# Performance work log

Hardware: AMD Instinct MI355X
Metric: run time of the kernel (lower is better)

## Reference

```python
import jax, jax.numpy as jnp
import numpy as np

N_NODES = 50000
N_EDGES = 400000
NUM_FEATS = 128
LATENT_DIM_Y = 64
HIDDEN = 512
OUT = 2


def gcn_conv(x, edge_index, W, b, num_nodes):
    """PyG GCNConv: add self-loops, symmetric normalization, x @ W then scatter-add."""
    x = x @ W  # [N, out_ch]
    loop = jnp.arange(num_nodes)
    row = jnp.concatenate([edge_index[0], loop])  # source nodes
    col = jnp.concatenate([edge_index[1], loop])  # target nodes
    deg = jax.ops.segment_sum(jnp.ones_like(col, dtype=x.dtype), col, num_segments=num_nodes)
    dinv = jnp.where(deg > 0, jax.lax.rsqrt(deg), 0.0)
    norm = dinv[row] * dinv[col]  # [E+N]
    msgs = norm[:, None] * x[row]  # gather source features, scale
    out = jax.ops.segment_sum(msgs, col, num_segments=num_nodes)
    return out + b


def setup_inputs() -> dict:
    key = jax.random.key(0)
    k1, k2, k3, k4, k5, k6, k7 = jax.random.split(key, 7)
    in_ch = NUM_FEATS + LATENT_DIM_Y
    inputs = {
        "edge_index": jax.random.randint(k1, (2, N_EDGES), 0, N_NODES),
        "X": jax.random.normal(k2, (N_NODES, NUM_FEATS), dtype=jnp.float32),
        "u_Y": jax.random.normal(k3, (N_NODES, LATENT_DIM_Y), dtype=jnp.float32),
        "W1": jax.random.normal(k4, (in_ch, HIDDEN), dtype=jnp.float32) / np.sqrt(in_ch),
        "b1": jnp.zeros((HIDDEN,), dtype=jnp.float32),
        "W2": jax.random.normal(k5, (HIDDEN, OUT), dtype=jnp.float32) / np.sqrt(HIDDEN),
        "b2": jnp.zeros((OUT,), dtype=jnp.float32),
    }
    return inputs


def reference(edge_index, X, u_Y, W1, b1, W2, b2):
    latent = jnp.concatenate([u_Y, X], axis=1)  # [N, latent+feats]
    h = jax.nn.relu(gcn_conv(latent, edge_index, W1, b1, N_NODES))
    y = gcn_conv(h, edge_index, W2, b2, N_NODES)
    # nn.Softmax() on a 2D tensor defaults to dim=1
    return jax.nn.softmax(y, axis=1)
```

## Files before the change

kernel.cpp:

```cpp
#include <hip/hip_runtime.h>

#define N_NODES 50000
#define N_EDGES 400000
#define FEATS   128
#define LAT     64
#define IN_CH   192
#define HID     512
#define MB      64
#define CAP     32

#define E4       100000
#define SC_BLKS  391
#define CVT_BLKS 9375
#define W1_BLKS  384

typedef __attribute__((ext_vector_type(8))) short bf16x8;
typedef __attribute__((ext_vector_type(4))) float f32x4;

static inline int cdiv(int a, int b) { return (a + b - 1) / b; }

__device__ __forceinline__ unsigned short f2bf(float f) {
    unsigned int u = __float_as_uint(f);
    u = (u + 0x7fffu + ((u >> 16) & 1u)) >> 16;
    return (unsigned short)u;
}
__device__ __forceinline__ float bf_lo(unsigned int u) {
    return __uint_as_float(u << 16);
}
__device__ __forceinline__ float bf_hi(unsigned int u) {
    return __uint_as_float(u & 0xffff0000u);
}

__global__ __launch_bounds__(256) void
k_front(const int* __restrict__ ei, int* __restrict__ cursor, int* __restrict__ csr_src,
        const float* __restrict__ uY, const float* __restrict__ X,
        unsigned short* __restrict__ latent,
        const float* __restrict__ W1, unsigned short* __restrict__ W1f) {
    int bid = blockIdx.x;
    if (bid < SC_BLKS) {
        int i4 = bid * 256 + threadIdx.x;
        if (i4 < E4) {
            int4 r = ((const int4*)ei)[i4];
            int4 c = ((const int4*)(ei + N_EDGES))[i4];
            int p0 = atomicAdd(&cursor[c.x], 1);
            int p1 = atomicAdd(&cursor[c.y], 1);
            int p2 = atomicAdd(&cursor[c.z], 1);
            int p3 = atomicAdd(&cursor[c.w], 1);
            csr_src[c.x * CAP + p0] = r.x;
            csr_src[c.y * CAP + p1] = r.y;
            csr_src[c.z * CAP + p2] = r.z;
            csr_src[c.w * CAP + p3] = r.w;
        }
    } else if (bid < SC_BLKS + CVT_BLKS) {
        int idx = (bid - SC_BLKS) * 256 + threadIdx.x;
        int i = idx / 48, q = idx % 48;
        const float4* uY4 = (const float4*)uY;
        const float4* X4  = (const float4*)X;
        float4 v = (q < LAT / 4) ? uY4[i * (LAT / 4) + q]
                                 : X4[i * (FEATS / 4) + (q - LAT / 4)];
        uint2 o;
        o.x = (unsigned int)f2bf(v.x) | ((unsigned int)f2bf(v.y) << 16);
        o.y = (unsigned int)f2bf(v.z) | ((unsigned int)f2bf(v.w) << 16);
        ((uint2*)latent)[idx] = o;
    } else {
        int idx = (bid - SC_BLKS - CVT_BLKS) * 256 + threadIdx.x;
        if (idx < IN_CH * HID) {
            int k = idx / HID, n = idx % HID;
            int ntile = n >> 4, nn = n & 15;
            int kc = k >> 5, q = (k >> 3) & 3, j = k & 7;
            int dst = (((ntile * 6 + kc) * 64 + q * 16 + nn) << 3) + j;
            W1f[dst] = f2bf(W1[idx]);
        }
    }
}

__device__ __forceinline__ void load_row(uint4* a, const uint4* __restrict__ L4,
                                         int r, int l8) {
    const uint4* p = L4 + (size_t)r * 24 + l8 * 3;
    a[0] = p[0]; a[1] = p[1]; a[2] = p[2];
}
__device__ __forceinline__ void fma_row(float* acc, const uint4* a, float wt) {
#pragma unroll
    for (int i = 0; i < 3; ++i) {
        unsigned int u0 = a[i].x, u1 = a[i].y, u2 = a[i].z, u3 = a[i].w;
        acc[i * 8 + 0] = fmaf(wt, bf_lo(u0), acc[i * 8 + 0]);
        acc[i * 8 + 1] = fmaf(wt, bf_hi(u0), acc[i * 8 + 1]);
        acc[i * 8 + 2] = fmaf(wt, bf_lo(u1), acc[i * 8 + 2]);
        acc[i * 8 + 3] = fmaf(wt, bf_hi(u1), acc[i * 8 + 3]);
        acc[i * 8 + 4] = fmaf(wt, bf_lo(u2), acc[i * 8 + 4]);
        acc[i * 8 + 5] = fmaf(wt, bf_hi(u2), acc[i * 8 + 5]);
        acc[i * 8 + 6] = fmaf(wt, bf_lo(u3), acc[i * 8 + 6]);
        acc[i * 8 + 7] = fmaf(wt, bf_hi(u3), acc[i * 8 + 7]);
    }
}

__global__ __launch_bounds__(256) void
k_gather_agg(const int* __restrict__ cursor, const int* __restrict__ csr_src,
             const unsigned short* __restrict__ latent, unsigned short* __restrict__ agg) {
    int w    = blockIdx.x * 4 + (threadIdx.x >> 6);
    int lane = threadIdx.x & 63;
    if (w >= N_NODES) return;
    int qt = lane >> 3, l8 = lane & 7;
    const uint4* __restrict__ L4 = (const uint4*)latent;

    int jlo = w * CAP;
    int deg  = cursor[w];
    int rawe = csr_src[jlo + max(qt - 1, 0)];
    int raw2 = csr_src[jlo + qt + 7];
    int raw1 = (qt == 0) ? w : rawe;
    int r1 = min(max(raw1, 0), N_NODES - 1);
    int r2 = min(max(raw2, 0), N_NODES - 1);
    int d1 = cursor[r1];
    int d2 = cursor[r2];

    uint4 a[3];
    load_row(a, L4, r1, l8);

    float di = rsqrtf((float)(deg + 1));
    float w1 = (qt == 0) ? di
             : ((qt - 1 < deg) ? rsqrtf((float)(d1 + 1)) : 0.f);

    float acc[24];
#pragma unroll
    for (int i = 0; i < 24; ++i) acc[i] = 0.f;

    bool more = (deg > 7);
    uint4 b[3];
    if (more) load_row(b, L4, r2, l8);

    fma_row(acc, a, w1);
    if (more) {
        float w2 = (qt + 7 < deg) ? rsqrtf((float)(d2 + 1)) : 0.f;
        fma_row(acc, b, w2);
        for (int e = 15 + qt; e < deg; e += 8) {
            int r = csr_src[jlo + e];
            float wt = rsqrtf((float)(cursor[r] + 1));
            uint4 t[3];
            load_row(t, L4, r, l8);
            fma_row(acc, t, wt);
        }
    }

#pragma unroll
    for (int i = 0; i < 24; ++i) {
        acc[i] += __shfl_xor(acc[i], 8);
        acc[i] += __shfl_xor(acc[i], 16);
        acc[i] += __shfl_xor(acc[i], 32);
    }

    if (qt == 0) {
        uint4* op = (uint4*)agg + (size_t)w * 24 + l8 * 3;
#pragma unroll
        for (int v = 0; v < 3; ++v) {
            uint4 o;
            o.x = (unsigned int)f2bf(di * acc[v * 8 + 0]) |
                  ((unsigned int)f2bf(di * acc[v * 8 + 1]) << 16);
            o.y = (unsigned int)f2bf(di * acc[v * 8 + 2]) |
                  ((unsigned int)f2bf(di * acc[v * 8 + 3]) << 16);
            o.z = (unsigned int)f2bf(di * acc[v * 8 + 4]) |
                  ((unsigned int)f2bf(di * acc[v * 8 + 5]) << 16);
            o.w = (unsigned int)f2bf(di * acc[v * 8 + 6]) |
                  ((unsigned int)f2bf(di * acc[v * 8 + 7]) << 16);
            op[v] = o;
        }
    }
}

__global__ __launch_bounds__(256, 2) void
k_gemm_mfma(const unsigned short* __restrict__ agg, const unsigned short* __restrict__ W1f,
            const float* __restrict__ b1, const float* __restrict__ W2,
            float* __restrict__ y_pre) {
    __shared__ unsigned short Af[MB * IN_CH];
    __shared__ float red[4][MB][2];

    int t  = threadIdx.x;
    int m0 = blockIdx.x * MB;

    {
        const uint4* src = (const uint4*)agg;
        for (int idx = t; idx < MB * 24; idx += 256) {
            int row = idx / 24, c = idx % 24;
            int g = m0 + row;
            uint4 v = make_uint4(0u, 0u, 0u, 0u);
            if (g < N_NODES) v = src[(size_t)g * 24 + c];
            int mt = row >> 4, m = row & 15, kc = c >> 2, q = c & 3;
            ((uint4*)Af)[(mt * 6 + kc) * 64 + q * 16 + m] = v;
        }
    }
    __syncthreads();

    int wid = t >> 6, lane = t & 63;
    int nl = lane & 15, q = lane >> 4;

    float b1v[8], w2a[8], w2b[8];
#pragma unroll
    for (int nt = 0; nt < 8; ++nt) {
        int n = wid * 128 + nt * 16 + nl;
        b1v[nt] = b1[n];
        w2a[nt] = W2[n * 2 + 0];
        w2b[nt] = W2[n * 2 + 1];
    }

    f32x4 acc[4][8];
#pragma unroll
    for (int mt = 0; mt < 4; ++mt)
#pragma unroll
        for (int nt = 0; nt < 8; ++nt) acc[mt][nt] = (f32x4){0.f, 0.f, 0.f, 0.f};

    const bf16x8* Afv = (const bf16x8*)Af;
    const bf16x8* Bv  = (const bf16x8*)W1f;
#pragma unroll
    for (int kc = 0; kc < 6; ++kc) {
        bf16x8 a[4];
#pragma unroll
        for (int mt = 0; mt < 4; ++mt) a[mt] = Afv[(mt * 6 + kc) * 64 + lane];
#pragma unroll
        for (int nt = 0; nt < 8; ++nt) {
            bf16x8 b = Bv[((wid * 8 + nt) * 6 + kc) * 64 + lane];
#pragma unroll
            for (int mt = 0; mt < 4; ++mt)
                acc[mt][nt] = __builtin_amdgcn_mfma_f32_16x16x32_bf16(a[mt], b, acc[mt][nt], 0, 0, 0);
        }
    }

#pragma unroll
    for (int mt = 0; mt < 4; ++mt) {
#pragma unroll
        for (int r = 0; r < 4; ++r) {
            float p0 = 0.f, p1 = 0.f;
#pragma unroll
            for (int nt = 0; nt < 8; ++nt) {
                float h = fmaxf(acc[mt][nt][r] + b1v[nt], 0.f);
                p0 = fmaf(h, w2a[nt], p0);
                p1 = fmaf(h, w2b[nt], p1);
            }
#pragma unroll
            for (int off = 1; off < 16; off <<= 1) {
                p0 += __shfl_xor(p0, off);
                p1 += __shfl_xor(p1, off);
            }
            if (nl == 0) {
                int row = mt * 16 + q * 4 + r;
                red[wid][row][0] = p0;
                red[wid][row][1] = p1;
            }
        }
    }
    __syncthreads();
    if (t < MB * 2) {
        int row = t >> 1, j = t & 1;
        float s = red[0][row][j] + red[1][row][j] + red[2][row][j] + red[3][row][j];
        int g = m0 + row;
        if (g < N_NODES) y_pre[g * 2 + j] = s;
    }
}

__global__ __launch_bounds__(256) void
k_gather_y(const int* __restrict__ cursor, const int* __restrict__ csr_src,
           const float* __restrict__ y_pre, const float* __restrict__ b2,
           float* __restrict__ out) {
    int i  = blockIdx.x * 32 + (threadIdx.x >> 3);
    int l8 = threadIdx.x & 7;
    if (i >= N_NODES) return;
    const float2* __restrict__ yp = (const float2*)y_pre;

    int jlo = i * CAP;
    int deg  = cursor[i];
    int rawe = csr_src[jlo + max(l8 - 1, 0)];
    int raw2 = csr_src[jlo + l8 + 7];
    int raw1 = (l8 == 0) ? i : rawe;
    int r1 = min(max(raw1, 0), N_NODES - 1);
    int r2 = min(max(raw2, 0), N_NODES - 1);
    int d1 = cursor[r1], d2 = cursor[r2];
    float2 v1 = yp[r1];

    float di = rsqrtf((float)(deg + 1));
    float w1 = (l8 == 0) ? di
             : ((l8 - 1 < deg) ? rsqrtf((float)(d1 + 1)) : 0.f);
    float a0 = w1 * v1.x, a1 = w1 * v1.y;
    if (deg > 7) {
        float2 v2 = yp[r2];
        float w2 = (l8 + 7 < deg) ? rsqrtf((float)(d2 + 1)) : 0.f;
        a0 = fmaf(w2, v2.x, a0);
        a1 = fmaf(w2, v2.y, a1);
        for (int e = 15 + l8; e < deg; e += 8) {
            int r = csr_src[jlo + e];
            float wt = rsqrtf((float)(cursor[r] + 1));
            float2 v = yp[r];
            a0 = fmaf(wt, v.x, a0);
            a1 = fmaf(wt, v.y, a1);
        }
    }
#pragma unroll
    for (int off = 1; off < 8; off <<= 1) {
        a0 += __shfl_xor(a0, off);
        a1 += __shfl_xor(a1, off);
    }
    if (l8 == 0) {
        float ya = di * a0 + b2[0];
        float yb = di * a1 + b2[1];
        float mx = fmaxf(ya, yb);
        float e0 = expf(ya - mx);
        float e1 = expf(yb - mx);
        float inv = 1.0f / (e0 + e1);
        out[i * 2 + 0] = e0 * inv;
        out[i * 2 + 1] = e1 * inv;
    }
}


extern "C" void kernel_launch(void* const* d_in, const int* in_sizes, int n_in,
                              void* d_out, int out_size, void* d_ws, size_t ws_size,
                              hipStream_t stream) {
    const int*   ei = (const int*)d_in[0];
    const float* X  = (const float*)d_in[1];
    const float* uY = (const float*)d_in[2];
    const float* W1 = (const float*)d_in[3];
    const float* b1 = (const float*)d_in[4];
    const float* W2 = (const float*)d_in[5];
    const float* b2 = (const float*)d_in[6];
    float* out = (float*)d_out;

    char* ws = (char*)d_ws;
    auto carve = [&](size_t bytes) {
        char* p = ws;
        ws += (bytes + 255) & ~size_t(255);
        return p;
    };
    int*   cursor    = (int*)carve(N_NODES * sizeof(int));
    int*   csr_src   = (int*)carve((size_t)N_NODES * CAP * sizeof(int));
    unsigned short* latent = (unsigned short*)carve((size_t)N_NODES * IN_CH * 2);
    unsigned short* aggb   = (unsigned short*)carve((size_t)N_NODES * IN_CH * 2);
    unsigned short* W1f    = (unsigned short*)carve((size_t)IN_CH * HID * 2);
    float* y_pre     = (float*)carve((size_t)N_NODES * 2 * sizeof(float));

    hipMemsetAsync(cursor, 0, N_NODES * sizeof(int), stream);

    k_front     <<<SC_BLKS + CVT_BLKS + W1_BLKS, 256, 0, stream>>>(
                      ei, cursor, csr_src, uY, X, latent, W1, W1f);

    k_gather_agg<<<cdiv(N_NODES, 4), 256, 0, stream>>>(
                      cursor, csr_src, latent, aggb);

    k_gemm_mfma <<<cdiv(N_NODES, MB), 256, 0, stream>>>(aggb, W1f, b1, W2, y_pre);

    k_gather_y  <<<cdiv(N_NODES, 32), 256, 0, stream>>>(
                      cursor, csr_src, y_pre, b2, out);
}
```

Measured before the change: 186.9 us.

## Restructure neighbor aggregation as two half-wave streams with prefetched dword loads

The gather-aggregate kernel drops the layout of 8 lane-groups, each loading 3 uint4 per neighbor row. Instead each half-wave of 32 lanes reads a whole 192-feature row as coalesced dwords, and the two halves walk alternate neighbors. Neighbor indices and normalization weights are loaded once per lane and broadcast with shuffles, and the next row is prefetched while the current one is accumulated. This cuts the cross-lane reduction from 72 shuffles to 6, lowers register use and folds the destination scale into the edge weights. The cost is a longer serial chain of neighbor steps per half-wave, with narrower loads in flight per lane.

After: 175.6 us. 1.06x faster.

```diff
diff --git a/kernel.cpp b/kernel.cpp
--- a/kernel.cpp
+++ b/kernel.cpp
@@ -23,6 +23,9 @@
     unsigned int u = __float_as_uint(f);
     u = (u + 0x7fffu + ((u >> 16) & 1u)) >> 16;
     return (unsigned short)u;
+}
+__device__ __forceinline__ unsigned int pack2bf(float lo, float hi) {
+    return (unsigned int)f2bf(lo) | ((unsigned int)f2bf(hi) << 16);
 }
 __device__ __forceinline__ float bf_lo(unsigned int u) {
     return __uint_as_float(u << 16);
@@ -59,8 +62,8 @@
         float4 v = (q < LAT / 4) ? uY4[i * (LAT / 4) + q]
                                  : X4[i * (FEATS / 4) + (q - LAT / 4)];
         uint2 o;
-        o.x = (unsigned int)f2bf(v.x) | ((unsigned int)f2bf(v.y) << 16);
-        o.y = (unsigned int)f2bf(v.z) | ((unsigned int)f2bf(v.w) << 16);
+        o.x = pack2bf(v.x, v.y);
+        o.y = pack2bf(v.z, v.w);
         ((uint2*)latent)[idx] = o;
     } else {
         int idx = (bid - SC_BLKS - CVT_BLKS) * 256 + threadIdx.x;
@@ -74,95 +77,67 @@
     }
 }
 
-__device__ __forceinline__ void load_row(uint4* a, const uint4* __restrict__ L4,
-                                         int r, int l8) {
-    const uint4* p = L4 + (size_t)r * 24 + l8 * 3;
-    a[0] = p[0]; a[1] = p[1]; a[2] = p[2];
-}
-__device__ __forceinline__ void fma_row(float* acc, const uint4* a, float wt) {
-#pragma unroll
-    for (int i = 0; i < 3; ++i) {
-        unsigned int u0 = a[i].x, u1 = a[i].y, u2 = a[i].z, u3 = a[i].w;
-        acc[i * 8 + 0] = fmaf(wt, bf_lo(u0), acc[i * 8 + 0]);
-        acc[i * 8 + 1] = fmaf(wt, bf_hi(u0), acc[i * 8 + 1]);
-        acc[i * 8 + 2] = fmaf(wt, bf_lo(u1), acc[i * 8 + 2]);
-        acc[i * 8 + 3] = fmaf(wt, bf_hi(u1), acc[i * 8 + 3]);
-        acc[i * 8 + 4] = fmaf(wt, bf_lo(u2), acc[i * 8 + 4]);
-        acc[i * 8 + 5] = fmaf(wt, bf_hi(u2), acc[i * 8 + 5]);
-        acc[i * 8 + 6] = fmaf(wt, bf_lo(u3), acc[i * 8 + 6]);
-        acc[i * 8 + 7] = fmaf(wt, bf_hi(u3), acc[i * 8 + 7]);
-    }
-}
-
 __global__ __launch_bounds__(256) void
 k_gather_agg(const int* __restrict__ cursor, const int* __restrict__ csr_src,
              const unsigned short* __restrict__ latent, unsigned short* __restrict__ agg) {
     int w    = blockIdx.x * 4 + (threadIdx.x >> 6);
     int lane = threadIdx.x & 63;
     if (w >= N_NODES) return;
-    int qt = lane >> 3, l8 = lane & 7;
-    const uint4* __restrict__ L4 = (const uint4*)latent;
-
-    int jlo = w * CAP;
-    int deg  = cursor[w];
-    int rawe = csr_src[jlo + max(qt - 1, 0)];
-    int raw2 = csr_src[jlo + qt + 7];
-    int raw1 = (qt == 0) ? w : rawe;
-    int r1 = min(max(raw1, 0), N_NODES - 1);
-    int r2 = min(max(raw2, 0), N_NODES - 1);
-    int d1 = cursor[r1];
-    int d2 = cursor[r2];
-
-    uint4 a[3];
-    load_row(a, L4, r1, l8);
-
+    int h  = lane >> 5;
+    int il = lane & 31;
+    const unsigned int* __restrict__ L = (const unsigned int*)latent;
+
+    int deg = cursor[w];
+    int raw = csr_src[w * CAP + max(il - 1, 0)];
+    int rl  = (il == 0) ? w : min(max(raw, 0), N_NODES - 1);
+    int dl  = cursor[rl];
     float di = rsqrtf((float)(deg + 1));
-    float w1 = (qt == 0) ? di
-             : ((qt - 1 < deg) ? rsqrtf((float)(d1 + 1)) : 0.f);
-
-    float acc[24];
-#pragma unroll
-    for (int i = 0; i < 24; ++i) acc[i] = 0.f;
-
-    bool more = (deg > 7);
-    uint4 b[3];
-    if (more) load_row(b, L4, r2, l8);
-
-    fma_row(acc, a, w1);
-    if (more) {
-        float w2 = (qt + 7 < deg) ? rsqrtf((float)(d2 + 1)) : 0.f;
-        fma_row(acc, b, w2);
-        for (int e = 15 + qt; e < deg; e += 8) {
-            int r = csr_src[jlo + e];
-            float wt = rsqrtf((float)(cursor[r] + 1));
-            uint4 t[3];
-            load_row(t, L4, r, l8);
-            fma_row(acc, t, wt);
-        }
-    }
-
-#pragma unroll
-    for (int i = 0; i < 24; ++i) {
-        acc[i] += __shfl_xor(acc[i], 8);
-        acc[i] += __shfl_xor(acc[i], 16);
-        acc[i] += __shfl_xor(acc[i], 32);
-    }
-
-    if (qt == 0) {
-        uint4* op = (uint4*)agg + (size_t)w * 24 + l8 * 3;
-#pragma unroll
-        for (int v = 0; v < 3; ++v) {
-            uint4 o;
-            o.x = (unsigned int)f2bf(di * acc[v * 8 + 0]) |
-                  ((unsigned int)f2bf(di * acc[v * 8 + 1]) << 16);
-            o.y = (unsigned int)f2bf(di * acc[v * 8 + 2]) |
-                  ((unsigned int)f2bf(di * acc[v * 8 + 3]) << 16);
-            o.z = (unsigned int)f2bf(di * acc[v * 8 + 4]) |
-                  ((unsigned int)f2bf(di * acc[v * 8 + 5]) << 16);
-            o.w = (unsigned int)f2bf(di * acc[v * 8 + 6]) |
-                  ((unsigned int)f2bf(di * acc[v * 8 + 7]) << 16);
-            op[v] = o;
-        }
+    float wl = (il == 0) ? di * di
+             : ((il - 1 < deg) ? di * rsqrtf((float)(dl + 1)) : 0.f);
+
+    int T = deg + 1;
+    int iters = (T + 1) >> 1;
+
+    float acc[6];
+#pragma unroll
+    for (int i = 0; i < 6; ++i) acc[i] = 0.f;
+
+    int   t  = h;
+    int   r0 = __shfl(rl, t);
+    float w0 = __shfl(wl, t);
+    {
+        const unsigned int* p = L + (size_t)r0 * 96 + il;
+        unsigned int a0 = p[0], b0 = p[32], c0 = p[64];
+        for (int it = 1; it < iters; ++it) {
+            int   t1 = t + 2;
+            int   r1 = __shfl(rl, t1);
+            float w1 = __shfl(wl, t1);
+            const unsigned int* q = L + (size_t)r1 * 96 + il;
+            unsigned int a1 = q[0], b1 = q[32], c1 = q[64];
+            acc[0] = fmaf(w0, bf_lo(a0), acc[0]);
+            acc[1] = fmaf(w0, bf_hi(a0), acc[1]);
+            acc[2] = fmaf(w0, bf_lo(b0), acc[2]);
+            acc[3] = fmaf(w0, bf_hi(b0), acc[3]);
+            acc[4] = fmaf(w0, bf_lo(c0), acc[4]);
+            acc[5] = fmaf(w0, bf_hi(c0), acc[5]);
+            t = t1; w0 = w1; a0 = a1; b0 = b1; c0 = c1;
+        }
+        acc[0] = fmaf(w0, bf_lo(a0), acc[0]);
+        acc[1] = fmaf(w0, bf_hi(a0), acc[1]);
+        acc[2] = fmaf(w0, bf_lo(b0), acc[2]);
+        acc[3] = fmaf(w0, bf_hi(b0), acc[3]);
+        acc[4] = fmaf(w0, bf_lo(c0), acc[4]);
+        acc[5] = fmaf(w0, bf_hi(c0), acc[5]);
+    }
+
+#pragma unroll
+    for (int i = 0; i < 6; ++i) acc[i] += __shfl_xor(acc[i], 32);
+
+    if (h == 0) {
+        unsigned int* op = (unsigned int*)agg + (size_t)w * 96 + il;
+        op[0]  = pack2bf(acc[0], acc[1]);
+        op[32] = pack2bf(acc[2], acc[3]);
+        op[64] = pack2bf(acc[4], acc[5]);
     }
 }
 
```
